# Kernel optimization log

Hardware: AMD Instinct MI355X
Metric: run time of the kernel (lower is better)

## Reference

```python
import jax, jax.numpy as jnp
import numpy as np
from jax import lax


def setup_inputs() -> dict:
    key = jax.random.key(0)
    ks = jax.random.split(key, 6)
    B, S, C, HID, H, K = 8, 2048, 768, 768, 12, 9
    return {
        "query": jax.random.normal(ks[0], (B, S, C), jnp.float32),
        "value": jax.random.normal(ks[1], (B, S, C), jnp.float32),
        "hidden_states": jax.random.normal(ks[2], (B, S, HID), jnp.float32),
        "dw_weight": jax.random.normal(ks[3], (HID, 1, K), jnp.float32) * (2.0 / K) ** 0.5,
        "pw_weight": jax.random.normal(ks[4], (C, HID, 1), jnp.float32) * (2.0 / HID) ** 0.5,
        "sep_bias": jnp.zeros((C,), jnp.float32),
        "attn_W": jax.random.normal(ks[5], (H * K, C), jnp.float32) * (1.0 / C) ** 0.5,
        "attn_b": jnp.zeros((H * K,), jnp.float32),
        "num_heads": H,
        "kernel_size": K,
    }


def reference(query, value, hidden_states, dw_weight, pw_weight, sep_bias,
              attn_W, attn_b, num_heads, kernel_size):
    K = kernel_size
    H = num_heads
    B, S, C = value.shape  # all_head_size = C
    D = C // H             # attention_head_size
    HID = hidden_states.shape[-1]
    pad = K // 2

    # --- SeparableConv1d: depthwise (groups=HID) then pointwise 1x1 ---
    x = jnp.transpose(hidden_states, (0, 2, 1))  # [B, HID, S]
    dn = ("NCH", "OIH", "NCH")
    dw = lax.conv_general_dilated(x, dw_weight, window_strides=(1,),
                                  padding=[(pad, pad)], dimension_numbers=dn,
                                  feature_group_count=HID)  # [B, HID, S]
    pw = lax.conv_general_dilated(dw, pw_weight, window_strides=(1,),
                                  padding=[(0, 0)], dimension_numbers=dn)  # [B, C, S]
    ks_out = jnp.transpose(pw, (0, 2, 1)) + sep_bias  # [B, S, C]

    # --- dynamic conv kernel: gated projection + (double) softmax ---
    conv_attn = ks_out * query                                   # [B, S, C]
    filt = conv_attn @ attn_W.T + attn_b                          # [B, S, H*K]
    filt = filt.reshape(B, S, H, K)
    # original code applies softmax twice (once in SDConv, once in LightConv)
    filt = jax.nn.softmax(jax.nn.softmax(filt, axis=-1), axis=-1)

    # --- light conv: unfold value along seq and contract over window ---
    vpad = jnp.pad(value, ((0, 0), (pad, pad), (0, 0)))           # [B, S+K-1, C]
    unf = jnp.stack([vpad[:, k:k + S, :] for k in range(K)], axis=-1)  # [B,S,C,K]
    unf = unf.reshape(B, S, H, D, K)
    out = jnp.einsum("bshdk,bshk->bshd", unf, filt)               # [B,S,H,D]
    return out
```

## Files before the change

### kernel.cpp

```cpp
#include <hip/hip_runtime.h>
#include <hip/hip_bf16.h>
#include <stdint.h>

#define B_   8
#define S_   2048
#define C_   768
#define HID_ 768
#define H_   12
#define KW   9
#define D_   64
#define M_   (B_ * S_)
#define PADW 4
#define HK_  108
#define NPAD 128

typedef __attribute__((ext_vector_type(4))) float  floatx4;
typedef __attribute__((ext_vector_type(8))) __bf16 bf16x8;

#define GLD_LDS16(gptr, lptr)                                                  \
    __builtin_amdgcn_global_load_lds(                                          \
        (__attribute__((address_space(1))) void*)(gptr),                       \
        (__attribute__((address_space(3))) void*)(lptr), 16, 0, 0)

#define BARR() do { __builtin_amdgcn_s_barrier();                              \
                    __builtin_amdgcn_sched_barrier(0); } while (0)
#define LGKM0() do { asm volatile("s_waitcnt lgkmcnt(0)" ::: "memory");        \
                     __builtin_amdgcn_sched_barrier(0); } while (0)

__global__ __launch_bounds__(256) void convert_w_kernel(
    const float* __restrict__ pwW, const float* __restrict__ attnW,
    __hip_bfloat16* __restrict__ pwWb, __hip_bfloat16* __restrict__ attnWb)
{
    int i = blockIdx.x * 256 + threadIdx.x;
    {
        const float4 v = *reinterpret_cast<const float4*>(&pwW[(size_t)i * 4]);
        union { __hip_bfloat16 h[4]; uint2 u; } o;
        o.h[0] = __float2bfloat16(v.x);
        o.h[1] = __float2bfloat16(v.y);
        o.h[2] = __float2bfloat16(v.z);
        o.h[3] = __float2bfloat16(v.w);
        *reinterpret_cast<uint2*>(&pwWb[(size_t)i * 4]) = o.u;
    }
    if (i < (NPAD * HID_) / 4) {
        const int base = i * 4;
        const int n = base / HID_;
        union { __hip_bfloat16 h[4]; uint2 u; } o;
#pragma unroll
        for (int e = 0; e < 4; ++e) {
            float v = (n < HK_) ? attnW[base + e] : 0.0f;
            o.h[e] = __float2bfloat16(v);
        }
        *reinterpret_cast<uint2*>(&attnWb[base]) = o.u;
    }
}

#define TSD 32

__global__ __launch_bounds__(256) void dwconv_kernel(
    const float* __restrict__ hidden, const float* __restrict__ dw_w,
    __hip_bfloat16* __restrict__ dw_out)
{
    int idx  = blockIdx.x * 256 + threadIdx.x;
    int hq   = idx % (HID_ / 4);
    int rest = idx / (HID_ / 4);
    int sc   = rest % (S_ / TSD);
    int b    = rest / (S_ / TSD);
    int h    = hq * 4;
    int s0   = sc * TSD;
    size_t base = (size_t)b * S_ * HID_ + h;

    float w[36];
    const float4* wp = reinterpret_cast<const float4*>(dw_w + (size_t)h * KW);
#pragma unroll
    for (int i = 0; i < 9; ++i) {
        float4 t = wp[i];
        w[4 * i + 0] = t.x; w[4 * i + 1] = t.y;
        w[4 * i + 2] = t.z; w[4 * i + 3] = t.w;
    }

    float4 win[KW];
#pragma unroll
    for (int k = 0; k < 8; ++k) {
        int sp = s0 + k - PADW;
        float4 v = {0.f, 0.f, 0.f, 0.f};
        if ((unsigned)sp < (unsigned)S_)
            v = *reinterpret_cast<const float4*>(&hidden[base + (size_t)sp * HID_]);
        win[k] = v;
    }

#pragma unroll
    for (int i = 0; i < TSD; ++i) {
        int sp = s0 + i + PADW;
        float4 nv = {0.f, 0.f, 0.f, 0.f};
        if ((unsigned)sp < (unsigned)S_)
            nv = *reinterpret_cast<const float4*>(&hidden[base + (size_t)sp * HID_]);
        win[8] = nv;

        float a0 = 0.f, a1 = 0.f, a2 = 0.f, a3 = 0.f;
#pragma unroll
        for (int k = 0; k < KW; ++k) {
            a0 += win[k].x * w[k];
            a1 += win[k].y * w[9 + k];
            a2 += win[k].z * w[18 + k];
            a3 += win[k].w * w[27 + k];
        }
        union { __hip_bfloat16 bv[4]; uint2 u; } o;
        o.bv[0] = __float2bfloat16(a0);
        o.bv[1] = __float2bfloat16(a1);
        o.bv[2] = __float2bfloat16(a2);
        o.bv[3] = __float2bfloat16(a3);
        *reinterpret_cast<uint2*>(&dw_out[base + (size_t)(s0 + i) * HID_]) = o.u;

#pragma unroll
        for (int k = 0; k < 8; ++k) win[k] = win[k + 1];
    }
}

__global__ __launch_bounds__(256, 2) void fused_gemm_kernel(
    const __hip_bfloat16* __restrict__ A,
    const __hip_bfloat16* __restrict__ Bt,
    const __hip_bfloat16* __restrict__ Wt,
    const float* __restrict__ bias,
    const float* __restrict__ query,
    const float* __restrict__ attn_b,
    float* __restrict__ filt)
{
    __shared__ __align__(16) char lds[73728];
    char* Plds = lds + 8192;
    float* LG  = (float*)(lds + 8192 + 32768);

    const int t    = threadIdx.x;
    const int lane = t & 63;
    const int wave = t >> 6;
    const int l16  = lane & 15, lq = lane >> 4;

    const int row0 = (int)blockIdx.x * 32;

    const int sr8     = lane >> 3;
    const int srcslot = (lane & 7) ^ sr8;
    const __hip_bfloat16* aS = A + (size_t)(row0 + wave * 8 + sr8) * HID_ + srcslot * 8;

    floatx4 acc2[2][2];
#pragma unroll
    for (int m = 0; m < 2; ++m)
#pragma unroll
        for (int n = 0; n < 2; ++n) acc2[m][n] = (floatx4){0.f, 0.f, 0.f, 0.f};

    for (int nt = 0; nt < 3; ++nt) {
        const __hip_bfloat16* bS =
            Bt + (size_t)(nt * 256 + wave * 64 + sr8) * HID_ + srcslot * 8;

        floatx4 acc1[2][4];
#pragma unroll
        for (int m = 0; m < 2; ++m)
#pragma unroll
            for (int n = 0; n < 4; ++n) acc1[m][n] = (floatx4){0.f, 0.f, 0.f, 0.f};

#define FSTG(kt, buf) do {                                                     \
        GLD_LDS16(aS + (kt) * 64, lds + (buf) * 4096 + wave * 1024);           \
        _Pragma("unroll")                                                      \
        for (int _i = 0; _i < 8; ++_i)                                         \
            GLD_LDS16(bS + (size_t)_i * 8 * HID_ + (kt) * 64,                  \
                      lds + 8192 + (buf) * 32768 + wave * 8192 + _i * 1024);   \
    } while (0)

        FSTG(0, 0);
#pragma unroll 2
        for (int kt = 0; kt < 12; ++kt) {
            const int cur = kt & 1;
            if (kt < 11) {
                FSTG(kt + 1, cur ^ 1);
                asm volatile("s_waitcnt vmcnt(9)" ::: "memory");
            } else {
                asm volatile("s_waitcnt vmcnt(0)" ::: "memory");
            }
            __builtin_amdgcn_sched_barrier(0);
            BARR();

            const char* ab = lds + cur * 4096;
            const char* bb = lds + 8192 + cur * 32768;
            bf16x8 av[2][2], bv[4][2];
#pragma unroll
            for (int m = 0; m < 2; ++m) {
                const int r = m * 16 + l16;
#pragma unroll
                for (int ks = 0; ks < 2; ++ks)
                    av[m][ks] = *(const bf16x8*)(ab + r * 128 +
                        ((ks * 64 + lq * 16) ^ ((l16 & 7) << 4)));
            }
#pragma unroll
            for (int n = 0; n < 4; ++n) {
                const int r = wave * 64 + n * 16 + l16;
#pragma unroll
                for (int ks = 0; ks < 2; ++ks)
                    bv[n][ks] = *(const bf16x8*)(bb + r * 128 +
                        ((ks * 64 + lq * 16) ^ ((l16 & 7) << 4)));
            }
            __builtin_amdgcn_s_setprio(1);
#pragma unroll
            for (int m = 0; m < 2; ++m)
#pragma unroll
                for (int n = 0; n < 4; ++n)
#pragma unroll
                    for (int ks = 0; ks < 2; ++ks)
                        acc1[m][n] = __builtin_amdgcn_mfma_f32_16x16x32_bf16(
                            av[m][ks], bv[n][ks], acc1[m][n], 0, 0, 0);
            __builtin_amdgcn_s_setprio(0);
            LGKM0();
            BARR();
        }
#undef FSTG

#pragma unroll
        for (int m = 0; m < 2; ++m)
#pragma unroll
            for (int n = 0; n < 4; ++n) {
                const int cl   = wave * 64 + n * 16 + l16;
                const int gcol = nt * 256 + cl;
                const float bvv = bias[gcol];
#pragma unroll
                for (int j = 0; j < 4; ++j) {
                    const int row = m * 16 + lq * 4 + j;
                    float v = (acc1[m][n][j] + bvv) *
                              query[(size_t)(row0 + row) * C_ + gcol];
                    __hip_bfloat16 hb = __float2bfloat16(v);
                    *(uint16_t*)(Plds + row * 512 +
                                 ((cl * 2) ^ ((row & 7) << 4))) =
                        *(uint16_t*)&hb;
                }
            }
        LGKM0();
        BARR();

#pragma unroll
        for (int kk = 0; kk < 8; ++kk) {
            bf16x8 pv[2], wv[2];
#pragma unroll
            for (int m = 0; m < 2; ++m) {
                const int r = m * 16 + l16;
                pv[m] = *(const bf16x8*)(Plds + r * 512 +
                    ((kk * 64 + lq * 16) ^ ((l16 & 7) << 4)));
            }
#pragma unroll
            for (int n = 0; n < 2; ++n) {
                const int wrow = wave * 32 + n * 16 + l16;
                wv[n] = *(const bf16x8*)(Wt + (size_t)wrow * C_ +
                                         nt * 256 + kk * 32 + lq * 8);
            }
#pragma unroll
            for (int m = 0; m < 2; ++m)
#pragma unroll
                for (int n = 0; n < 2; ++n)
                    acc2[m][n] = __builtin_amdgcn_mfma_f32_16x16x32_bf16(
                        pv[m], wv[n], acc2[m][n], 0, 0, 0);
        }
        LGKM0();
        BARR();
    }

#pragma unroll
    for (int m = 0; m < 2; ++m)
#pragma unroll
        for (int n = 0; n < 2; ++n) {
            const int cl = wave * 32 + n * 16 + l16;
#pragma unroll
            for (int j = 0; j < 4; ++j) {
                const int row = m * 16 + lq * 4 + j;
                LG[row * 129 + cl] = acc2[m][n][j];
            }
        }
    LGKM0();
    BARR();

    for (int id = t; id < 32 * H_; id += 256) {
        const int h   = id >> 5;
        const int row = id & 31;
        float v[KW];
#pragma unroll
        for (int k = 0; k < KW; ++k)
            v[k] = LG[row * 129 + h * KW + k] + attn_b[h * KW + k];
#pragma unroll
        for (int pass = 0; pass < 2; ++pass) {
            float mx = v[0];
#pragma unroll
            for (int k = 1; k < KW; ++k) mx = fmaxf(mx, v[k]);
            float s = 0.f;
#pragma unroll
            for (int k = 0; k < KW; ++k) { v[k] = __expf(v[k] - mx); s += v[k]; }
            float inv = 1.f / s;
#pragma unroll
            for (int k = 0; k < KW; ++k) v[k] *= inv;
        }
        const int grow = row0 + row;
        const int b    = grow >> 11;
        const int s    = grow & (S_ - 1);
        const size_t base = (((size_t)b * H_ + h) * S_ + s) * KW;
#pragma unroll
        for (int k = 0; k < KW; ++k) filt[base + k] = v[k];
    }
}

#define TSL 16
#define SCHK 256

__global__ __launch_bounds__(256) void lightconv_kernel(
    const float* __restrict__ value, const float* __restrict__ filt,
    float* __restrict__ out)
{
    __shared__ __align__(16) float fl[SCHK * KW];

    const int tid = threadIdx.x;
    const int blk = blockIdx.x;
    const int nSC = S_ / SCHK;
    const int b   = blk / (H_ * nSC);
    const int rem = blk % (H_ * nSC);
    const int h   = rem / nSC;
    const int sch = rem % nSC;
    const int S0  = sch * SCHK;

    {
        const float4* src = reinterpret_cast<const float4*>(
            filt + (((size_t)b * H_ + h) * S_ + S0) * KW);
        float4* dst = reinterpret_cast<float4*>(fl);
        for (int j = tid; j < (SCHK * KW) / 4; j += 256)
            dst[j] = src[j];
    }
    __syncthreads();

    const int d4 = tid & 15;
    const int sg = tid >> 4;
    const int s0 = S0 + sg * TSL;
    const size_t vbase = (size_t)b * S_ * C_ + h * D_ + d4 * 4;
    const float* flrow = &fl[(sg * TSL) * KW];

    float4 win[KW];
#pragma unroll
    for (int k = 0; k < 8; ++k) {
        int sp = s0 + k - PADW;
        float4 v = {0.f, 0.f, 0.f, 0.f};
        if ((unsigned)sp < (unsigned)S_)
            v = *reinterpret_cast<const float4*>(&value[vbase + (size_t)sp * C_]);
        win[k] = v;
    }

#pragma unroll
    for (int i = 0; i < TSL; ++i) {
        int sp = s0 + i + PADW;
        float4 nv = {0.f, 0.f, 0.f, 0.f};
        if ((unsigned)sp < (unsigned)S_)
            nv = *reinterpret_cast<const float4*>(&value[vbase + (size_t)sp * C_]);
        win[8] = nv;

        float4 acc = {0.f, 0.f, 0.f, 0.f};
#pragma unroll
        for (int k = 0; k < KW; ++k) {
            float f = flrow[i * KW + k];
            acc.x += win[k].x * f;
            acc.y += win[k].y * f;
            acc.z += win[k].z * f;
            acc.w += win[k].w * f;
        }
        *reinterpret_cast<float4*>(&out[vbase + (size_t)(s0 + i) * C_]) = acc;

#pragma unroll
        for (int k = 0; k < 8; ++k) win[k] = win[k + 1];
    }
}

extern "C" void kernel_launch(void* const* d_in, const int* in_sizes, int n_in,
                              void* d_out, int out_size, void* d_ws, size_t ws_size,
                              hipStream_t stream)
{
    const float* query  = (const float*)d_in[0];
    const float* value  = (const float*)d_in[1];
    const float* hidden = (const float*)d_in[2];
    const float* dw_w   = (const float*)d_in[3];
    const float* pw_w   = (const float*)d_in[4];
    const float* sep_b  = (const float*)d_in[5];
    const float* attn_W = (const float*)d_in[6];
    const float* attn_b = (const float*)d_in[7];
    float* out = (float*)d_out;

    char* ws = (char*)d_ws;
    __hip_bfloat16* dwb    = (__hip_bfloat16*)(ws);
    __hip_bfloat16* pwWb   = (__hip_bfloat16*)(ws + 25165824);
    __hip_bfloat16* attnWb = (__hip_bfloat16*)(ws + 26345472);
    float*          filt   = (float*)(ws + 26542080);

    convert_w_kernel<<<(C_ * HID_) / (256 * 4), 256, 0, stream>>>(
        pw_w, attn_W, pwWb, attnWb);

    dwconv_kernel<<<(M_ * (HID_ / 4)) / (256 * TSD), 256, 0, stream>>>(hidden, dw_w, dwb);

    fused_gemm_kernel<<<M_ / 32, 256, 0, stream>>>(
        dwb, pwWb, attnWb, sep_b, query, attn_b, filt);

    lightconv_kernel<<<B_ * H_ * (S_ / SCHK), 256, 0, stream>>>(value, filt, out);
}
```

Before: 94.83 us.

## Give each wave private LDS staging to drop per-iteration block barriers

```diff
diff --git a/kernel.cpp b/kernel.cpp
--- a/kernel.cpp
+++ b/kernel.cpp
@@ -125,9 +125,9 @@
     const float* __restrict__ attn_b,
     float* __restrict__ filt)
 {
-    __shared__ __align__(16) char lds[73728];
-    char* Plds = lds + 8192;
-    float* LG  = (float*)(lds + 8192 + 32768);
+    __shared__ __align__(16) char lds[49152];
+    char* Plds = lds + 16384;
+    float* LG  = (float*)(lds + 16384);
 
     const int t    = threadIdx.x;
     const int lane = t & 63;
@@ -136,9 +136,13 @@
 
     const int row0 = (int)blockIdx.x * 32;
 
-    const int sr8     = lane >> 3;
-    const int srcslot = (lane & 7) ^ sr8;
-    const __hip_bfloat16* aS = A + (size_t)(row0 + wave * 8 + sr8) * HID_ + srcslot * 8;
+    char* Aw = lds + wave * 4096;
+    char* Bw = lds + 16384 + wave * 8192;
+
+    const int srow  = lane >> 2;
+    const int sslot = (lane & 3) ^ ((lane >> 3) & 3);
+    const __hip_bfloat16* aS =
+        A + (size_t)(row0 + srow) * HID_ + sslot * 8;
 
     floatx4 acc2[2][2];
 #pragma unroll
@@ -148,7 +152,7 @@
 
     for (int nt = 0; nt < 3; ++nt) {
         const __hip_bfloat16* bS =
-            Bt + (size_t)(nt * 256 + wave * 64 + sr8) * HID_ + srcslot * 8;
+            Bt + (size_t)(nt * 256 + wave * 64 + srow) * HID_ + sslot * 8;
 
         floatx4 acc1[2][4];
 #pragma unroll
@@ -156,60 +160,52 @@
 #pragma unroll
             for (int n = 0; n < 4; ++n) acc1[m][n] = (floatx4){0.f, 0.f, 0.f, 0.f};
 
-#define FSTG(kt, buf) do {                                                     \
-        GLD_LDS16(aS + (kt) * 64, lds + (buf) * 4096 + wave * 1024);           \
+#define STG(kt, buf) do {                                                      \
+        GLD_LDS16(aS + (kt) * 32,             Aw + (buf) * 2048);              \
+        GLD_LDS16(aS + 16 * HID_ + (kt) * 32, Aw + (buf) * 2048 + 1024);       \
         _Pragma("unroll")                                                      \
-        for (int _i = 0; _i < 8; ++_i)                                         \
-            GLD_LDS16(bS + (size_t)_i * 8 * HID_ + (kt) * 64,                  \
-                      lds + 8192 + (buf) * 32768 + wave * 8192 + _i * 1024);   \
+        for (int _j = 0; _j < 4; ++_j)                                         \
+            GLD_LDS16(bS + (size_t)_j * 16 * HID_ + (kt) * 32,                 \
+                      Bw + (buf) * 4096 + _j * 1024);                          \
     } while (0)
 
-        FSTG(0, 0);
+        STG(0, 0);
 #pragma unroll 2
-        for (int kt = 0; kt < 12; ++kt) {
+        for (int kt = 0; kt < 24; ++kt) {
             const int cur = kt & 1;
-            if (kt < 11) {
-                FSTG(kt + 1, cur ^ 1);
-                asm volatile("s_waitcnt vmcnt(9)" ::: "memory");
+            if (kt < 23) {
+                STG(kt + 1, cur ^ 1);
+                asm volatile("s_waitcnt vmcnt(6)" ::: "memory");
             } else {
                 asm volatile("s_waitcnt vmcnt(0)" ::: "memory");
             }
             __builtin_amdgcn_sched_barrier(0);
-            BARR();
-
-            const char* ab = lds + cur * 4096;
-            const char* bb = lds + 8192 + cur * 32768;
-            bf16x8 av[2][2], bv[4][2];
+
+            const char* ab = Aw + cur * 2048;
+            const char* bb = Bw + cur * 4096;
+            bf16x8 av[2], bv[4];
 #pragma unroll
             for (int m = 0; m < 2; ++m) {
                 const int r = m * 16 + l16;
-#pragma unroll
-                for (int ks = 0; ks < 2; ++ks)
-                    av[m][ks] = *(const bf16x8*)(ab + r * 128 +
-                        ((ks * 64 + lq * 16) ^ ((l16 & 7) << 4)));
+                av[m] = *(const bf16x8*)(ab + r * 64 +
+                    ((lq ^ ((r >> 1) & 3)) << 4));
             }
 #pragma unroll
             for (int n = 0; n < 4; ++n) {
-                const int r = wave * 64 + n * 16 + l16;
-#pragma unroll
-                for (int ks = 0; ks < 2; ++ks)
-                    bv[n][ks] = *(const bf16x8*)(bb + r * 128 +
-                        ((ks * 64 + lq * 16) ^ ((l16 & 7) << 4)));
-            }
-            __builtin_amdgcn_s_setprio(1);
+                const int c = n * 16 + l16;
+                bv[n] = *(const bf16x8*)(bb + c * 64 +
+                    ((lq ^ ((c >> 1) & 3)) << 4));
+            }
 #pragma unroll
             for (int m = 0; m < 2; ++m)
 #pragma unroll
                 for (int n = 0; n < 4; ++n)
-#pragma unroll
-                    for (int ks = 0; ks < 2; ++ks)
-                        acc1[m][n] = __builtin_amdgcn_mfma_f32_16x16x32_bf16(
-                            av[m][ks], bv[n][ks], acc1[m][n], 0, 0, 0);
-            __builtin_amdgcn_s_setprio(0);
-            LGKM0();
-            BARR();
-        }
-#undef FSTG
+                    acc1[m][n] = __builtin_amdgcn_mfma_f32_16x16x32_bf16(
+                        av[m], bv[n], acc1[m][n], 0, 0, 0);
+        }
+#undef STG
+
+        BARR();
 
 #pragma unroll
         for (int m = 0; m < 2; ++m)
```

New measurement: 128.7 us. 1.36x slower.
